# Kernel optimization log

Measured on AMD Instinct MI355X. Metric: run time of the kernel, lower is better.

The kernel has to match this reference:

```python
import jax, jax.numpy as jnp
import numpy as np

B, T, C = 64, 256, 1024
H, DH = 16, 64           # n_heads, head_dim (C == H*DH)
NP, WS = 16, 2           # n_patches per side, window_size (T == NP*NP)
EPS = 1e-5


def setup_inputs() -> dict:
    key = jax.random.key(0)
    ks = jax.random.split(key, 8)
    s = lambda k, shape, fan: jax.random.normal(k, shape, jnp.float32) * (fan ** -0.5)
    return dict(
        x=jax.random.normal(ks[0], (B, T, C), jnp.float32),
        ln1_g=jnp.ones((C,), jnp.float32), ln1_b=jnp.zeros((C,), jnp.float32),
        Wq=s(ks[1], (H, C, DH), C), Wk=s(ks[2], (H, C, DH), C), Wv=s(ks[3], (H, C, DH), C),
        Wp=s(ks[4], (C, C), C), bp=jnp.zeros((C,), jnp.float32),
        ln2_g=jnp.ones((C,), jnp.float32), ln2_b=jnp.zeros((C,), jnp.float32),
        W1=s(ks[5], (C, C), C), b1=jnp.zeros((C,), jnp.float32),
        W2=s(ks[6], (C, C), C), b2=jnp.zeros((C,), jnp.float32))


def _ln(x, g, b):
    m = x.mean(-1, keepdims=True)
    v = x.var(-1, keepdims=True)
    return (x - m) * jax.lax.rsqrt(v + EPS) * g + b


def reference(x, ln1_g, ln1_b, Wq, Wk, Wv, Wp, bp, ln2_g, ln2_b, W1, b1, W2, b2):
    h = NP // WS                      # windows per side = 8
    nw = h * h                        # 64 windows of WS*WS = 4 tokens
    xn = _ln(x, ln1_g, ln1_b)
    # window partition: [B, T, C] -> [B*nw, WS*WS, C]
    xw = (xn.reshape(B, h, WS, h, WS, C)
            .transpose(0, 1, 3, 2, 4, 5)
            .reshape(B * nw, WS * WS, C))
    # all-heads batched QKV (original loops over heads; math identical since
    # torch.cat of per-head outputs == head-axis stack then reshape)
    q = jnp.einsum('ntc,hcd->nhtd', xw, Wq)
    k = jnp.einsum('ntc,hcd->nhtd', xw, Wk)
    v = jnp.einsum('ntc,hcd->nhtd', xw, Wv)
    # NOTE: scale is C**-0.5 with C = d_model (faithful to source, not head_dim)
    wei = jax.nn.softmax(jnp.einsum('nhqd,nhkd->nhqk', q, k) * (C ** -0.5), axis=-1)
    att = jnp.einsum('nhqk,nhkd->nhqd', wei, v)
    att = att.transpose(0, 2, 1, 3).reshape(B * nw, WS * WS, C)
    att = att @ Wp + bp
    # residual adds the LayerNorm-ed, window-partitioned x (faithful quirk)
    xr = xw + att
    # reverse window partition -> [B, T, C]
    xr = (xr.reshape(B, h, h, WS, WS, C)
            .transpose(0, 1, 3, 2, 4, 5)
            .reshape(B, T, C))
    ff = jax.nn.gelu(_ln(xr, ln2_g, ln2_b) @ W1 + b1, approximate=False) @ W2 + b2
    return xr + ff
```

## Files before the change

kernel.cpp:

```cpp
#include <hip/hip_runtime.h>
#include <math.h>

typedef unsigned short u16;
typedef unsigned int   u32;

using f32x4  = __attribute__((ext_vector_type(4))) float;
using s16x8  = __attribute__((ext_vector_type(8))) short;
using u16x8  = __attribute__((ext_vector_type(8))) unsigned short;

__device__ __forceinline__ u16 f2b(float f) {
    u32 u = __float_as_uint(f);
    u += 0x7FFFu + ((u >> 16) & 1u);
    return (u16)(u >> 16);
}
__device__ __forceinline__ float b2f(u16 u) { return __uint_as_float(((u32)u) << 16); }

__device__ __forceinline__ int natrow(int R) {
    int b = R >> 8, r8 = R & 255, w = r8 >> 2, t = r8 & 3;
    return (b << 8) + ((((w >> 3) << 1) + (t >> 1)) << 4) + ((w & 7) << 1) + (t & 1);
}

__device__ __forceinline__ void gll16(const void* g, void* l) {
    __builtin_amdgcn_global_load_lds(
        (const __attribute__((address_space(1))) void*)g,
        (__attribute__((address_space(3))) void*)l, 16, 0, 0);
}

__device__ __forceinline__ void transpose_body(
    const float* __restrict__ in, u16* __restrict__ out, int R, int C)
{
    __shared__ float tile[32][33];
    const int tx = threadIdx.x, ty = threadIdx.y;
    const int c  = blockIdx.x * 32 + tx;
    const int r0 = blockIdx.y * 32;
#pragma unroll
    for (int i = 0; i < 32; i += 8) tile[ty + i][tx] = in[(size_t)(r0 + ty + i) * C + c];
    __syncthreads();
    const int orow0 = blockIdx.x * 32;
    const int ocol  = r0 + tx;
#pragma unroll
    for (int i = 0; i < 32; i += 8)
        out[(size_t)(orow0 + ty + i) * R + ocol] = f2b(tile[tx][ty + i]);
}

__global__ __launch_bounds__(256) void transpose_qkv(
    const float* __restrict__ Wq, const float* __restrict__ Wk,
    const float* __restrict__ Wv, u16* __restrict__ out)
{
    const int z = blockIdx.z;
    const float* in = (z < 16 ? Wq : z < 32 ? Wk : Wv) + (size_t)(z & 15) * 65536;
    transpose_body(in, out + (size_t)z * 65536, 1024, 64);
}

__global__ __launch_bounds__(256) void transpose_pw(
    const float* __restrict__ Wp, const float* __restrict__ W1,
    const float* __restrict__ W2, u16* __restrict__ out)
{
    const int z = blockIdx.z;
    const float* in = z == 0 ? Wp : z == 1 ? W1 : W2;
    transpose_body(in, out + (size_t)z * 1048576, 1024, 1024);
}

template<int MAP, int BIN>
__global__ __launch_bounds__(256) void ln_kernel(
    const void* __restrict__ X, const float* __restrict__ g, const float* __restrict__ bta,
    u16* __restrict__ outB)
{
    const int R   = blockIdx.x;
    const int src = MAP ? natrow(R) : R;
    float x0, x1, x2, x3;
    if (BIN) {
        const ushort4 r = ((const ushort4*)((const u16*)X + (size_t)src * 1024))[threadIdx.x];
        x0 = b2f(r.x); x1 = b2f(r.y); x2 = b2f(r.z); x3 = b2f(r.w);
    } else {
        const float4 r = ((const float4*)((const float*)X + (size_t)src * 1024))[threadIdx.x];
        x0 = r.x; x1 = r.y; x2 = r.z; x3 = r.w;
    }
    float s  = x0 + x1 + x2 + x3;
    float s2 = x0 * x0 + x1 * x1 + x2 * x2 + x3 * x3;
#pragma unroll
    for (int o = 32; o; o >>= 1) { s += __shfl_xor(s, o); s2 += __shfl_xor(s2, o); }
    __shared__ float red[8];
    const int w = threadIdx.x >> 6, l = threadIdx.x & 63;
    if (l == 0) { red[w] = s; red[w + 4] = s2; }
    __syncthreads();
    s  = red[0] + red[1] + red[2] + red[3];
    s2 = red[4] + red[5] + red[6] + red[7];
    const float mean = s * (1.f / 1024.f);
    const float var  = s2 * (1.f / 1024.f) - mean * mean;
    const float rinv = rsqrtf(var + 1e-5f);
    const float4 gv = ((const float4*)g)[threadIdx.x];
    const float4 bv = ((const float4*)bta)[threadIdx.x];
    ((ushort4*)(outB + (size_t)R * 1024))[threadIdx.x] = make_ushort4(
        f2b((x0 - mean) * rinv * gv.x + bv.x), f2b((x1 - mean) * rinv * gv.y + bv.y),
        f2b((x2 - mean) * rinv * gv.z + bv.z), f2b((x3 - mean) * rinv * gv.w + bv.w));
}

template<int MODE>
__global__ __launch_bounds__(512, 2) void gemm256(
    const u16* __restrict__ A, const u16* __restrict__ Bt,
    const float* __restrict__ bias, const void* __restrict__ resid,
    void* __restrict__ Out, int M, int N, int K, int LDA, int NB)
{
    extern __shared__ char lds[];
    const int NT = K >> 6;
    const int nblk = gridDim.x;
    const int x = blockIdx.x & 7, i = blockIdx.x >> 3;
    const int R = (nblk >> 3) / NB;
    const int ncs = NB >> 2;
    const int sc = i >> 4, u = i & 15;
    const int scr = sc / ncs, scc = sc - scr * ncs;
    const int mb = x * R + scr * 4 + (u >> 2);
    const int nb = scc * 4 + (u & 3);
    const int row0 = mb * 256, col0 = nb * 256;
    const int tid = threadIdx.x;
    const int w = tid >> 6, l = tid & 63;
    const int wr = w >> 2, wc = w & 3;
    const int lr = l & 15, kg = l >> 4;
    const int xs = (lr & 7) << 4;
    const int koff[2] = { (kg * 16) ^ xs, (64 + kg * 16) ^ xs };
    const int abase_l = wr * 8192 + lr * 128;
    const int bbase_l = wc * 4096 + lr * 128;

    f32x4 acc[2][2][4][2] = {};
    s16x8 a0[4][2], a1[4][2], b0[2][2], b1[2][2];

    auto stage = [&](int ts, int item) {
        if (ts >= NT) return;
        const int d = ts & 1;
        const int isB = item & 1, h = item >> 1;
        char* lbase = lds + (isB ? 65536 : 0) + d * 32768 + h * 16384;
        const u16* gptr = isB ? Bt : A;
        const int ld = isB ? K : LDA;
        const int blk0 = (isB ? col0 : row0) + h * 128;
#pragma unroll
        for (int j = 0; j < 2; ++j) {
            const int p = j * 512 + tid;
            const int q = p ^ ((p >> 3) & 7);
            const int grow = blk0 + (q >> 3);
            const int gcol = ts * 64 + (q & 7) * 8;
            gll16(gptr + (size_t)grow * ld + gcol, lbase + (j * 8 + w) * 1024);
        }
    };

#define SB __builtin_amdgcn_sched_barrier(0)
#define LOAD_A(dst, qm) do { \
    _Pragma("unroll") for (int kk = 0; kk < 2; ++kk) \
    _Pragma("unroll") for (int i2 = 0; i2 < 4; ++i2) \
        dst[i2][kk] = *(const s16x8*)(Ab + (qm) * 16384 + abase_l + i2 * 2048 + koff[kk]); \
} while (0)
#define LOAD_B(dst, qn) do { \
    _Pragma("unroll") for (int kk = 0; kk < 2; ++kk) \
    _Pragma("unroll") for (int n = 0; n < 2; ++n) \
        dst[n][kk] = *(const s16x8*)(Bb + (qn) * 16384 + bbase_l + n * 2048 + koff[kk]); \
} while (0)
#define LGKM0 do { \
    asm volatile("s_waitcnt lgkmcnt(0)" ::: "memory"); SB; \
} while (0)
#define MFMA_Q(qm, qn, aa, bb) do { \
    __builtin_amdgcn_s_setprio(1); \
    _Pragma("unroll") for (int kk = 0; kk < 2; ++kk) \
    _Pragma("unroll") for (int i2 = 0; i2 < 4; ++i2) \
    _Pragma("unroll") for (int n = 0; n < 2; ++n) \
        acc[qm][qn][i2][n] = __builtin_amdgcn_mfma_f32_16x16x32_bf16( \
            aa[i2][kk], bb[n][kk], acc[qm][qn][i2][n], 0, 0, 0); \
    __builtin_amdgcn_s_setprio(0); SB; \
} while (0)
#define GATE(NSTR) do { \
    asm volatile("s_waitcnt vmcnt(" NSTR ")" ::: "memory"); \
    __builtin_amdgcn_s_barrier(); SB; \
} while (0)

    stage(0, 0); stage(0, 1); stage(0, 2); stage(0, 3);

    for (int t = 0; t < NT - 1; ++t) {
        const char* Ab = lds + (t & 1) * 32768;
        const char* Bb = lds + 65536 + (t & 1) * 32768;
        GATE("4");
        LOAD_A(a0, 0); LOAD_B(b0, 0); SB;
        stage(t + 1, 0); SB;
        LGKM0;
        MFMA_Q(0, 0, a0, b0);
        GATE("4");
        LOAD_A(a1, 1); SB;
        stage(t + 1, 1); SB;
        LGKM0;
        MFMA_Q(1, 0, a1, b0);
        GATE("4");
        LOAD_B(b1, 1); SB;
        stage(t + 1, 2); SB;
        LGKM0;
        MFMA_Q(1, 1, a1, b1);
        stage(t + 1, 3); SB;
        MFMA_Q(0, 1, a0, b1);
    }
    {
        const int t = NT - 1;
        const char* Ab = lds + (t & 1) * 32768;
        const char* Bb = lds + 65536 + (t & 1) * 32768;
        GATE("4");
        LOAD_A(a0, 0); LOAD_B(b0, 0); SB;
        LGKM0;
        MFMA_Q(0, 0, a0, b0);
        GATE("2");
        LOAD_A(a1, 1); SB;
        LGKM0;
        MFMA_Q(1, 0, a1, b0);
        GATE("0");
        LOAD_B(b1, 1); SB;
        LGKM0;
        MFMA_Q(1, 1, a1, b1);
        MFMA_Q(0, 1, a0, b1);
    }
#undef SB
#undef LOAD_A
#undef LOAD_B
#undef LGKM0
#undef MFMA_Q
#undef GATE

#pragma unroll
    for (int qm = 0; qm < 2; ++qm)
#pragma unroll
    for (int i2 = 0; i2 < 4; ++i2) {
        const int grb = row0 + qm * 128 + wr * 64 + i2 * 16 + kg * 4;
#pragma unroll
        for (int qn = 0; qn < 2; ++qn)
#pragma unroll
        for (int n = 0; n < 2; ++n) {
            const int gc = col0 + qn * 128 + wc * 32 + n * 16 + lr;
#pragma unroll
            for (int j = 0; j < 4; ++j) {
                const int gr = grb + j;
                const float v = acc[qm][qn][i2][n][j];
                if (MODE == 0) {
                    ((u16*)Out)[(size_t)gr * N + gc] = f2b(v);
                } else if (MODE == 2) {
                    const float tt = v + bias[gc];
                    ((u16*)Out)[(size_t)gr * N + gc] = f2b(0.5f * tt * (1.f + erff(tt * 0.70710678118f)));
                } else if (MODE == 3) {
                    ((float*)Out)[(size_t)natrow(gr) * N + gc] =
                        v + bias[gc] + b2f(((const u16*)resid)[(size_t)gr * N + gc]);
                } else {
                    ((u16*)Out)[(size_t)gr * N + gc] =
                        f2b(v + bias[gc] + b2f(((const u16*)resid)[(size_t)gr * N + gc]));
                }
            }
        }
    }
}

__global__ __launch_bounds__(256) void attn_kernel(u16* __restrict__ QKV)
{
    const int w = threadIdx.x >> 6, l = threadIdx.x & 63;
    const int n = blockIdx.x * 4 + w;
    u16* base = QKV + (size_t)n * 4 * 3072;
    const float scale = 0.03125f;
#pragma unroll
    for (int c = 0; c < 2; ++c) {
        const int col = c * 512 + l * 8;
        u16x8 qr[4], kr[4], vr[4];
#pragma unroll
        for (int t = 0; t < 4; ++t) {
            qr[t] = *(const u16x8*)(base + t * 3072 + col);
            kr[t] = *(const u16x8*)(base + t * 3072 + 1024 + col);
            vr[t] = *(const u16x8*)(base + t * 3072 + 2048 + col);
        }
        float qf[4][8], kf[4][8];
#pragma unroll
        for (int t = 0; t < 4; ++t)
#pragma unroll
            for (int j = 0; j < 8; ++j) { qf[t][j] = b2f(qr[t][j]); kf[t][j] = b2f(kr[t][j]); }
        float s[4][4];
#pragma unroll
        for (int t = 0; t < 4; ++t)
#pragma unroll
            for (int u = 0; u < 4; ++u) {
                float p = qf[t][0] * kf[u][0];
#pragma unroll
                for (int j = 1; j < 8; ++j) p += qf[t][j] * kf[u][j];
                p += __shfl_xor(p, 1); p += __shfl_xor(p, 2); p += __shfl_xor(p, 4);
                s[t][u] = p * scale;
            }
#pragma unroll
        for (int t = 0; t < 4; ++t) {
            const float m = fmaxf(fmaxf(s[t][0], s[t][1]), fmaxf(s[t][2], s[t][3]));
            const float e0 = expf(s[t][0] - m), e1 = expf(s[t][1] - m);
            const float e2 = expf(s[t][2] - m), e3 = expf(s[t][3] - m);
            const float inv = 1.f / (e0 + e1 + e2 + e3);
            u16x8 o;
#pragma unroll
            for (int j = 0; j < 8; ++j)
                o[j] = f2b((e0 * b2f(vr[0][j]) + e1 * b2f(vr[1][j]) +
                            e2 * b2f(vr[2][j]) + e3 * b2f(vr[3][j])) * inv);
            *(u16x8*)(base + t * 3072 + col) = o;
        }
    }
}

extern "C" void kernel_launch(void* const* d_in, const int* in_sizes, int n_in,
                              void* d_out, int out_size, void* d_ws, size_t ws_size,
                              hipStream_t stream)
{
    const float* x    = (const float*)d_in[0];
    const float* ln1g = (const float*)d_in[1];
    const float* ln1b = (const float*)d_in[2];
    const float* Wq   = (const float*)d_in[3];
    const float* Wk   = (const float*)d_in[4];
    const float* Wv   = (const float*)d_in[5];
    const float* Wp   = (const float*)d_in[6];
    const float* bp   = (const float*)d_in[7];
    const float* ln2g = (const float*)d_in[8];
    const float* ln2b = (const float*)d_in[9];
    const float* W1   = (const float*)d_in[10];
    const float* b1   = (const float*)d_in[11];
    const float* W2   = (const float*)d_in[12];
    const float* b2   = (const float*)d_in[13];
    float* out = (float*)d_out;

    char* ws = (char*)d_ws;
    const size_t MB = 1024 * 1024;
    u16* xr_b  = (u16*)ws;
    u16* xw_b  = (u16*)(ws + 32 * MB);
    u16* qkv   = (u16*)(ws + 64 * MB);
    u16* h1b   = (u16*)(ws + 64 * MB);
    u16* ln2bf = (u16*)(ws + 160 * MB);
    u16* WqkvT = (u16*)(ws + 192 * MB);
    u16* WpT   = (u16*)(ws + 198 * MB);
    u16* W1T   = WpT + (1u << 20);
    u16* W2T   = W1T + (1u << 20);

    hipFuncSetAttribute((const void*)gemm256<0>, hipFuncAttributeMaxDynamicSharedMemorySize, 131072);
    hipFuncSetAttribute((const void*)gemm256<2>, hipFuncAttributeMaxDynamicSharedMemorySize, 131072);
    hipFuncSetAttribute((const void*)gemm256<3>, hipFuncAttributeMaxDynamicSharedMemorySize, 131072);
    hipFuncSetAttribute((const void*)gemm256<5>, hipFuncAttributeMaxDynamicSharedMemorySize, 131072);

    const int M = 16384, K = 1024;
    dim3 tpb(32, 8);
    transpose_qkv<<<dim3(2, 32, 48), tpb, 0, stream>>>(Wq, Wk, Wv, WqkvT);
    transpose_pw <<<dim3(32, 32, 3), tpb, 0, stream>>>(Wp, W1, W2, WpT);

    ln_kernel<1, 0><<<16384, 256, 0, stream>>>(x, ln1g, ln1b, xw_b);

    gemm256<0><<<768, 512, 131072, stream>>>(xw_b, WqkvT, nullptr, nullptr, qkv, M, 3072, K, K, 12);

    attn_kernel<<<1024, 256, 0, stream>>>(qkv);

    gemm256<5><<<256, 512, 131072, stream>>>(qkv, WpT, bp, xw_b, xr_b, M, 1024, K, 3072, 4);

    ln_kernel<0, 1><<<16384, 256, 0, stream>>>(xr_b, ln2g, ln2b, ln2bf);

    gemm256<2><<<256, 512, 131072, stream>>>(ln2bf, W1T, b1, nullptr, h1b, M, 1024, K, K, 4);

    gemm256<3><<<256, 512, 131072, stream>>>(h1b, W2T, b2, xr_b, out, M, 1024, K, K, 4);
}
```

Baseline: 310.2 us.

## Restructure GEMM main loop with single barrier and fine-grained LDS/MFMA interleave

Rewrites the GEMM k-loop so each iteration waits once on global loads and one barrier, then issues all four next-stage async copies up front. LDS fragment reads are split per k-subslice and interleaved with MFMA groups using partial lgkmcnt waits. The peeled last iteration is folded into the loop. The aim is fewer barriers and better overlap of LDS reads with matrix math, at the cost of a coarser vmcnt(0) wait on the prefetched tile.

```diff
diff --git a/kernel.cpp b/kernel.cpp
--- a/kernel.cpp
+++ b/kernel.cpp
@@ -144,80 +144,56 @@
     };
 
 #define SB __builtin_amdgcn_sched_barrier(0)
-#define LOAD_A(dst, qm) do { \
-    _Pragma("unroll") for (int kk = 0; kk < 2; ++kk) \
+#define RDA(dst, qm, kk) do { \
     _Pragma("unroll") for (int i2 = 0; i2 < 4; ++i2) \
         dst[i2][kk] = *(const s16x8*)(Ab + (qm) * 16384 + abase_l + i2 * 2048 + koff[kk]); \
 } while (0)
-#define LOAD_B(dst, qn) do { \
-    _Pragma("unroll") for (int kk = 0; kk < 2; ++kk) \
+#define RDB(dst, qn, kk) do { \
     _Pragma("unroll") for (int n = 0; n < 2; ++n) \
         dst[n][kk] = *(const s16x8*)(Bb + (qn) * 16384 + bbase_l + n * 2048 + koff[kk]); \
 } while (0)
-#define LGKM0 do { \
-    asm volatile("s_waitcnt lgkmcnt(0)" ::: "memory"); SB; \
+#define WL(NS) do { \
+    asm volatile("s_waitcnt lgkmcnt(" NS ")" ::: "memory"); SB; \
 } while (0)
-#define MFMA_Q(qm, qn, aa, bb) do { \
-    __builtin_amdgcn_s_setprio(1); \
-    _Pragma("unroll") for (int kk = 0; kk < 2; ++kk) \
+#define M8(qm, qn, aa, bb, kk) do { \
     _Pragma("unroll") for (int i2 = 0; i2 < 4; ++i2) \
     _Pragma("unroll") for (int n = 0; n < 2; ++n) \
         acc[qm][qn][i2][n] = __builtin_amdgcn_mfma_f32_16x16x32_bf16( \
             aa[i2][kk], bb[n][kk], acc[qm][qn][i2][n], 0, 0, 0); \
-    __builtin_amdgcn_s_setprio(0); SB; \
+    SB; \
 } while (0)
-#define GATE(NSTR) do { \
-    asm volatile("s_waitcnt vmcnt(" NSTR ")" ::: "memory"); \
-    __builtin_amdgcn_s_barrier(); SB; \
-} while (0)
 
     stage(0, 0); stage(0, 1); stage(0, 2); stage(0, 3);
 
-    for (int t = 0; t < NT - 1; ++t) {
+    for (int t = 0; t < NT; ++t) {
         const char* Ab = lds + (t & 1) * 32768;
         const char* Bb = lds + 65536 + (t & 1) * 32768;
-        GATE("4");
-        LOAD_A(a0, 0); LOAD_B(b0, 0); SB;
-        stage(t + 1, 0); SB;
-        LGKM0;
-        MFMA_Q(0, 0, a0, b0);
-        GATE("4");
-        LOAD_A(a1, 1); SB;
-        stage(t + 1, 1); SB;
-        LGKM0;
-        MFMA_Q(1, 0, a1, b0);
-        GATE("4");
-        LOAD_B(b1, 1); SB;
-        stage(t + 1, 2); SB;
-        LGKM0;
-        MFMA_Q(1, 1, a1, b1);
-        stage(t + 1, 3); SB;
-        MFMA_Q(0, 1, a0, b1);
-    }
-    {
-        const int t = NT - 1;
-        const char* Ab = lds + (t & 1) * 32768;
-        const char* Bb = lds + 65536 + (t & 1) * 32768;
-        GATE("4");
-        LOAD_A(a0, 0); LOAD_B(b0, 0); SB;
-        LGKM0;
-        MFMA_Q(0, 0, a0, b0);
-        GATE("2");
-        LOAD_A(a1, 1); SB;
-        LGKM0;
-        MFMA_Q(1, 0, a1, b0);
-        GATE("0");
-        LOAD_B(b1, 1); SB;
-        LGKM0;
-        MFMA_Q(1, 1, a1, b1);
-        MFMA_Q(0, 1, a0, b1);
+        asm volatile("s_waitcnt vmcnt(0)" ::: "memory");
+        __builtin_amdgcn_s_barrier(); SB;
+        RDA(a0, 0, 0); RDB(b0, 0, 0); SB;
+        RDA(a0, 0, 1); RDB(b0, 0, 1); SB;
+        stage(t + 1, 0); stage(t + 1, 1); stage(t + 1, 2); stage(t + 1, 3);
+        SB;
+        __builtin_amdgcn_s_setprio(1);
+        WL("6");  M8(0, 0, a0, b0, 0);
+        RDA(a1, 1, 0); SB;
+        WL("4");  M8(0, 0, a0, b0, 1);
+        RDA(a1, 1, 1); SB;
+        WL("4");  M8(1, 0, a1, b0, 0);
+        RDB(b1, 1, 0); SB;
+        WL("2");  M8(1, 0, a1, b0, 1);
+        RDB(b1, 1, 1); SB;
+        WL("2");  M8(1, 1, a1, b1, 0);
+        WL("0");  M8(1, 1, a1, b1, 1);
+                  M8(0, 1, a0, b1, 0);
+                  M8(0, 1, a0, b1, 1);
+        __builtin_amdgcn_s_setprio(0); SB;
     }
 #undef SB
-#undef LOAD_A
-#undef LOAD_B
-#undef LGKM0
-#undef MFMA_Q
-#undef GATE
+#undef RDA
+#undef RDB
+#undef WL
+#undef M8
 
 #pragma unroll
     for (int qm = 0; qm < 2; ++qm)
@@ -330,10 +306,10 @@
     u16* W1T   = WpT + (1u << 20);
     u16* W2T   = W1T + (1u << 20);
 
-    hipFuncSetAttribute((const void*)gemm256<0>, hipFuncAttributeMaxDynamicSharedMemorySize, 131072);
-    hipFuncSetAttribute((const void*)gemm256<2>, hipFuncAttributeMaxDynamicSharedMemorySize, 131072);
-    hipFuncSetAttribute((const void*)gemm256<3>, hipFuncAttributeMaxDynamicSharedMemorySize, 131072);
-    hipFuncSetAttribute((const void*)gemm256<5>, hipFuncAttributeMaxDynamicSharedMemorySize, 131072);
+    (void)hipFuncSetAttribute((const void*)gemm256<0>, hipFuncAttributeMaxDynamicSharedMemorySize, 131072);
+    (void)hipFuncSetAttribute((const void*)gemm256<2>, hipFuncAttributeMaxDynamicSharedMemorySize, 131072);
+    (void)hipFuncSetAttribute((const void*)gemm256<3>, hipFuncAttributeMaxDynamicSharedMemorySize, 131072);
+    (void)hipFuncSetAttribute((const void*)gemm256<5>, hipFuncAttributeMaxDynamicSharedMemorySize, 131072);
 
     const int M = 16384, K = 1024;
     dim3 tpb(32, 8);
```

After: 312.2 us. About the same (+0.6%).

## Fuse QKV projection GEMM with windowed attention in one kernel

Applied to the files above, without the earlier changes.

Reorders the transposed QKV weights per head (q,k,v contiguous per head) so one 256x192 GEMM tile holds a head's Q, K and V for 256 tokens. A new kernel computes that tile, stages it in LDS as bf16, then runs the 4-token window softmax attention in-place and writes only the 1024-wide attention output. This removes the separate attention kernel and the round-trip of the 3072-wide QKV buffer through global memory. In exchange, the new GEMM has a simpler single-barrier pipeline and a different tile shape, which may use the MFMA units less efficiently than the tuned 256x256 kernel.

```diff
diff --git a/kernel.cpp b/kernel.cpp
--- a/kernel.cpp
+++ b/kernel.cpp
@@ -49,7 +49,8 @@
 {
     const int z = blockIdx.z;
     const float* in = (z < 16 ? Wq : z < 32 ? Wk : Wv) + (size_t)(z & 15) * 65536;
-    transpose_body(in, out + (size_t)z * 65536, 1024, 64);
+    const int h = z & 15, sec = z < 16 ? 0 : (z < 32 ? 1 : 2);
+    transpose_body(in, out + ((size_t)h * 192 + sec * 64) * 1024, 1024, 64);
 }
 
 __global__ __launch_bounds__(256) void transpose_pw(
@@ -94,6 +95,143 @@
     ((ushort4*)(outB + (size_t)R * 1024))[threadIdx.x] = make_ushort4(
         f2b((x0 - mean) * rinv * gv.x + bv.x), f2b((x1 - mean) * rinv * gv.y + bv.y),
         f2b((x2 - mean) * rinv * gv.z + bv.z), f2b((x3 - mean) * rinv * gv.w + bv.w));
+}
+
+__global__ __launch_bounds__(512, 2) void gemm_qkv_attn(
+    const u16* __restrict__ A, const u16* __restrict__ Bt,
+    u16* __restrict__ Att, int M, int K)
+{
+    extern __shared__ char lds[];
+    const int NT = K >> 6;
+    const int x = blockIdx.x & 7, i = blockIdx.x >> 3;
+    const int sc = i >> 4, u = i & 15;
+    const int scr = sc >> 2, scc = sc & 3;
+    const int mb = x * 8 + scr * 4 + (u >> 2);
+    const int nb = scc * 4 + (u & 3);
+    const int row0 = mb * 256, col0 = nb * 192;
+    const int tid = threadIdx.x;
+    const int w = tid >> 6, l = tid & 63;
+    const int wr = w & 3, wcg = w >> 2;
+    const int lr = l & 15, kg = l >> 4;
+    const int xs = (lr & 7) << 4;
+    const int koff[2] = { (kg * 16) ^ xs, (64 + kg * 16) ^ xs };
+    const int abase_l = wr * 8192 + lr * 128;
+    const int bbase_l = wcg * 12288 + lr * 128;
+
+    f32x4 acc[4][6] = {};
+    s16x8 a[4][2], b[6][2];
+
+    auto stageQ = [&](int ts) {
+        if (ts >= NT) return;
+        const int d = ts & 1, gcolb = ts * 64;
+        const int sl = (tid & 7) ^ ((tid >> 3) & 7);
+#pragma unroll
+        for (int h2 = 0; h2 < 2; ++h2)
+#pragma unroll
+            for (int j = 0; j < 2; ++j) {
+                const int c = j * 512 + tid;
+                const int s2 = (c & 7) ^ ((c >> 3) & 7);
+                gll16(A + (size_t)(row0 + h2 * 128 + (c >> 3)) * K + gcolb + s2 * 8,
+                      lds + d * 32768 + h2 * 16384 + (j * 8 + w) * 1024);
+            }
+#pragma unroll
+        for (int k2 = 0; k2 < 3; ++k2)
+            gll16(Bt + (size_t)(col0 + k2 * 64 + (tid >> 3)) * K + gcolb + sl * 8,
+                  lds + 65536 + d * 24576 + k2 * 8192 + w * 1024);
+    };
+
+#define SB __builtin_amdgcn_sched_barrier(0)
+#define WLq(NS) do { asm volatile("s_waitcnt lgkmcnt(" NS ")" ::: "memory"); SB; } while (0)
+
+    stageQ(0);
+
+    for (int t = 0; t < NT; ++t) {
+        const char* Ab = lds + (t & 1) * 32768 + abase_l;
+        const char* Bb = lds + 65536 + (t & 1) * 24576 + bbase_l;
+        asm volatile("s_waitcnt vmcnt(0)" ::: "memory");
+        __builtin_amdgcn_s_barrier(); SB;
+#pragma unroll
+        for (int i2 = 0; i2 < 4; ++i2) a[i2][0] = *(const s16x8*)(Ab + i2 * 2048 + koff[0]);
+#pragma unroll
+        for (int n = 0; n < 6; ++n)   b[n][0]  = *(const s16x8*)(Bb + n * 2048 + koff[0]);
+        SB;
+#pragma unroll
+        for (int i2 = 0; i2 < 4; ++i2) a[i2][1] = *(const s16x8*)(Ab + i2 * 2048 + koff[1]);
+#pragma unroll
+        for (int n = 0; n < 6; ++n)   b[n][1]  = *(const s16x8*)(Bb + n * 2048 + koff[1]);
+        SB;
+        stageQ(t + 1); SB;
+        __builtin_amdgcn_s_setprio(1);
+        WLq("10");
+#pragma unroll
+        for (int i2 = 0; i2 < 4; ++i2)
+#pragma unroll
+            for (int n = 0; n < 6; ++n)
+                acc[i2][n] = __builtin_amdgcn_mfma_f32_16x16x32_bf16(a[i2][0], b[n][0], acc[i2][n], 0, 0, 0);
+        SB;
+        WLq("0");
+#pragma unroll
+        for (int i2 = 0; i2 < 4; ++i2)
+#pragma unroll
+            for (int n = 0; n < 6; ++n)
+                acc[i2][n] = __builtin_amdgcn_mfma_f32_16x16x32_bf16(a[i2][1], b[n][1], acc[i2][n], 0, 0, 0);
+        __builtin_amdgcn_s_setprio(0); SB;
+    }
+#undef WLq
+
+    __builtin_amdgcn_s_barrier();
+    u16* attL = (u16*)lds;
+#pragma unroll
+    for (int i2 = 0; i2 < 4; ++i2)
+#pragma unroll
+        for (int n = 0; n < 6; ++n)
+#pragma unroll
+            for (int j = 0; j < 4; ++j)
+                attL[(wr * 64 + i2 * 16 + kg * 4 + j) * 200 + wcg * 96 + n * 16 + lr] =
+                    f2b(acc[i2][n][j]);
+    __builtin_amdgcn_s_barrier();
+
+    {
+        const int wl = tid >> 3, j = tid & 7;
+        const float scale = 0.03125f;
+        u16x8 qv[4], kv[4], vv[4];
+#pragma unroll
+        for (int t = 0; t < 4; ++t) {
+            qv[t] = *(const u16x8*)&attL[(wl * 4 + t) * 200 + j * 8];
+            kv[t] = *(const u16x8*)&attL[(wl * 4 + t) * 200 + 64 + j * 8];
+            vv[t] = *(const u16x8*)&attL[(wl * 4 + t) * 200 + 128 + j * 8];
+        }
+        float qf[4][8], kf[4][8];
+#pragma unroll
+        for (int t = 0; t < 4; ++t)
+#pragma unroll
+            for (int c = 0; c < 8; ++c) { qf[t][c] = b2f(qv[t][c]); kf[t][c] = b2f(kv[t][c]); }
+        float s[4][4];
+#pragma unroll
+        for (int t = 0; t < 4; ++t)
+#pragma unroll
+            for (int u2 = 0; u2 < 4; ++u2) {
+                float p = qf[t][0] * kf[u2][0];
+#pragma unroll
+                for (int c = 1; c < 8; ++c) p += qf[t][c] * kf[u2][c];
+                p += __shfl_xor(p, 1); p += __shfl_xor(p, 2); p += __shfl_xor(p, 4);
+                s[t][u2] = p * scale;
+            }
+#pragma unroll
+        for (int t = 0; t < 4; ++t) {
+            const float m = fmaxf(fmaxf(s[t][0], s[t][1]), fmaxf(s[t][2], s[t][3]));
+            const float e0 = expf(s[t][0] - m), e1 = expf(s[t][1] - m);
+            const float e2 = expf(s[t][2] - m), e3 = expf(s[t][3] - m);
+            const float inv = 1.f / (e0 + e1 + e2 + e3);
+            u16x8 o;
+#pragma unroll
+            for (int c = 0; c < 8; ++c)
+                o[c] = f2b((e0 * b2f(vv[0][c]) + e1 * b2f(vv[1][c]) +
+                            e2 * b2f(vv[2][c]) + e3 * b2f(vv[3][c])) * inv);
+            *(u16x8*)(Att + (size_t)(row0 + wl * 4 + t) * 1024 + nb * 64 + j * 8) = o;
+        }
+    }
+#undef SB
 }
 
 template<int MODE>
@@ -137,9 +275,8 @@
         for (int j = 0; j < 2; ++j) {
             const int p = j * 512 + tid;
             const int q = p ^ ((p >> 3) & 7);
-            const int grow = blk0 + (q >> 3);
-            const int gcol = ts * 64 + (q & 7) * 8;
-            gll16(gptr + (size_t)grow * ld + gcol, lbase + (j * 8 + w) * 1024);
+            gll16(gptr + (size_t)(blk0 + (q >> 3)) * ld + ts * 64 + (q & 7) * 8,
+                  lbase + (j * 8 + w) * 1024);
         }
     };
 
@@ -154,9 +291,7 @@
     _Pragma("unroll") for (int n = 0; n < 2; ++n) \
         dst[n][kk] = *(const s16x8*)(Bb + (qn) * 16384 + bbase_l + n * 2048 + koff[kk]); \
 } while (0)
-#define LGKM0 do { \
-    asm volatile("s_waitcnt lgkmcnt(0)" ::: "memory"); SB; \
-} while (0)
+#define LGKM0 do { asm volatile("s_waitcnt lgkmcnt(0)" ::: "memory"); SB; } while (0)
 #define MFMA_Q(qm, qn, aa, bb) do { \
     __builtin_amdgcn_s_setprio(1); \
     _Pragma("unroll") for (int kk = 0; kk < 2; ++kk) \
@@ -233,9 +368,7 @@
             for (int j = 0; j < 4; ++j) {
                 const int gr = grb + j;
                 const float v = acc[qm][qn][i2][n][j];
-                if (MODE == 0) {
-                    ((u16*)Out)[(size_t)gr * N + gc] = f2b(v);
-                } else if (MODE == 2) {
+                if (MODE == 2) {
                     const float tt = v + bias[gc];
                     ((u16*)Out)[(size_t)gr * N + gc] = f2b(0.5f * tt * (1.f + erff(tt * 0.70710678118f)));
                 } else if (MODE == 3) {
@@ -246,54 +379,6 @@
                         f2b(v + bias[gc] + b2f(((const u16*)resid)[(size_t)gr * N + gc]));
                 }
             }
-        }
-    }
-}
-
-__global__ __launch_bounds__(256) void attn_kernel(u16* __restrict__ QKV)
-{
-    const int w = threadIdx.x >> 6, l = threadIdx.x & 63;
-    const int n = blockIdx.x * 4 + w;
-    u16* base = QKV + (size_t)n * 4 * 3072;
-    const float scale = 0.03125f;
-#pragma unroll
-    for (int c = 0; c < 2; ++c) {
-        const int col = c * 512 + l * 8;
-        u16x8 qr[4], kr[4], vr[4];
-#pragma unroll
-        for (int t = 0; t < 4; ++t) {
-            qr[t] = *(const u16x8*)(base + t * 3072 + col);
-            kr[t] = *(const u16x8*)(base + t * 3072 + 1024 + col);
-            vr[t] = *(const u16x8*)(base + t * 3072 + 2048 + col);
-        }
-        float qf[4][8], kf[4][8];
-#pragma unroll
-        for (int t = 0; t < 4; ++t)
-#pragma unroll
-            for (int j = 0; j < 8; ++j) { qf[t][j] = b2f(qr[t][j]); kf[t][j] = b2f(kr[t][j]); }
-        float s[4][4];
-#pragma unroll
-        for (int t = 0; t < 4; ++t)
-#pragma unroll
-            for (int u = 0; u < 4; ++u) {
-                float p = qf[t][0] * kf[u][0];
-#pragma unroll
-                for (int j = 1; j < 8; ++j) p += qf[t][j] * kf[u][j];
-                p += __shfl_xor(p, 1); p += __shfl_xor(p, 2); p += __shfl_xor(p, 4);
-                s[t][u] = p * scale;
-            }
-#pragma unroll
-        for (int t = 0; t < 4; ++t) {
-            const float m = fmaxf(fmaxf(s[t][0], s[t][1]), fmaxf(s[t][2], s[t][3]));
-            const float e0 = expf(s[t][0] - m), e1 = expf(s[t][1] - m);
-            const float e2 = expf(s[t][2] - m), e3 = expf(s[t][3] - m);
-            const float inv = 1.f / (e0 + e1 + e2 + e3);
-            u16x8 o;
-#pragma unroll
-            for (int j = 0; j < 8; ++j)
-                o[j] = f2b((e0 * b2f(vr[0][j]) + e1 * b2f(vr[1][j]) +
-                            e2 * b2f(vr[2][j]) + e3 * b2f(vr[3][j])) * inv);
-            *(u16x8*)(base + t * 3072 + col) = o;
         }
     }
 }
@@ -322,18 +407,18 @@
     const size_t MB = 1024 * 1024;
     u16* xr_b  = (u16*)ws;
     u16* xw_b  = (u16*)(ws + 32 * MB);
-    u16* qkv   = (u16*)(ws + 64 * MB);
-    u16* h1b   = (u16*)(ws + 64 * MB);
-    u16* ln2bf = (u16*)(ws + 160 * MB);
+    u16* att   = (u16*)(ws + 64 * MB);
+    u16* h1b   = (u16*)(ws + 96 * MB);
+    u16* ln2bf = (u16*)(ws + 128 * MB);
     u16* WqkvT = (u16*)(ws + 192 * MB);
     u16* WpT   = (u16*)(ws + 198 * MB);
     u16* W1T   = WpT + (1u << 20);
     u16* W2T   = W1T + (1u << 20);
 
-    hipFuncSetAttribute((const void*)gemm256<0>, hipFuncAttributeMaxDynamicSharedMemorySize, 131072);
-    hipFuncSetAttribute((const void*)gemm256<2>, hipFuncAttributeMaxDynamicSharedMemorySize, 131072);
-    hipFuncSetAttribute((const void*)gemm256<3>, hipFuncAttributeMaxDynamicSharedMemorySize, 131072);
-    hipFuncSetAttribute((const void*)gemm256<5>, hipFuncAttributeMaxDynamicSharedMemorySize, 131072);
+    (void)hipFuncSetAttribute((const void*)gemm_qkv_attn, hipFuncAttributeMaxDynamicSharedMemorySize, 114688);
+    (void)hipFuncSetAttribute((const void*)gemm256<2>, hipFuncAttributeMaxDynamicSharedMemorySize, 131072);
+    (void)hipFuncSetAttribute((const void*)gemm256<3>, hipFuncAttributeMaxDynamicSharedMemorySize, 131072);
+    (void)hipFuncSetAttribute((const void*)gemm256<5>, hipFuncAttributeMaxDynamicSharedMemorySize, 131072);
 
     const int M = 16384, K = 1024;
     dim3 tpb(32, 8);
@@ -342,11 +427,9 @@
 
     ln_kernel<1, 0><<<16384, 256, 0, stream>>>(x, ln1g, ln1b, xw_b);
 
-    gemm256<0><<<768, 512, 131072, stream>>>(xw_b, WqkvT, nullptr, nullptr, qkv, M, 3072, K, K, 12);
-
-    attn_kernel<<<1024, 256, 0, stream>>>(qkv);
-
-    gemm256<5><<<256, 512, 131072, stream>>>(qkv, WpT, bp, xw_b, xr_b, M, 1024, K, 3072, 4);
+    gemm_qkv_attn<<<1024, 512, 114688, stream>>>(xw_b, WqkvT, att, M, K);
+
+    gemm256<5><<<256, 512, 131072, stream>>>(att, WpT, bp, xw_b, xr_b, M, 1024, K, K, 4);
 
     ln_kernel<0, 1><<<16384, 256, 0, stream>>>(xr_b, ln2g, ln2b, ln2bf);
 
```

After: 289.7 us. 6.6% less time.
